# Optimization experiments

Hardware: AMD Instinct MI355X
Metric: run time of the kernel (lower is better)

The kernel has to match this reference:

```python
import jax, jax.numpy as jnp
import numpy as np

D_MODEL = 1024
NUM_TILES = 64
TPC = 8                      # tiles_per_cluster
NUM_CLUSTERS = NUM_TILES // TPC
GRID = 16
COMP_H = 256                 # compress hidden = d_model // 4
NUM_KNOTS = 8
EPS_LN = 1e-5


def setup_inputs() -> dict:
    key = jax.random.key(0)
    ks = jax.random.split(key, 12)
    B, T = 4, 4096
    x = jax.random.normal(ks[0], (B, T, D_MODEL), dtype=jnp.float32)
    signatures_raw = jax.random.normal(ks[1], (NUM_TILES, D_MODEL), dtype=jnp.float32) * 0.5
    knot_values = jax.nn.sigmoid(jnp.linspace(-3.0, 3.0, NUM_KNOTS).astype(jnp.float32))
    temperature = jnp.ones((1,), dtype=jnp.float32)
    # compress: Linear(d,comp_h) -> GELU -> Linear(comp_h,2) -> Tanh
    compress_w1 = jax.random.normal(ks[2], (D_MODEL, COMP_H), dtype=jnp.float32) * (1.0 / np.sqrt(D_MODEL))
    compress_b1 = jnp.zeros((COMP_H,), dtype=jnp.float32)
    compress_w2 = jax.random.normal(ks[3], (COMP_H, 2), dtype=jnp.float32) * (1.0 / np.sqrt(COMP_H))
    compress_b2 = jnp.zeros((2,), dtype=jnp.float32)
    # per-tile magnitude splines: Linear(2,grid) -> ReLU -> Linear(grid,1)
    spline_w1 = jax.random.normal(ks[4], (NUM_TILES, 2, GRID), dtype=jnp.float32) * (1.0 / np.sqrt(2.0))
    spline_b1 = jnp.zeros((NUM_TILES, GRID), dtype=jnp.float32)
    spline_w2 = jax.random.normal(ks[5], (NUM_TILES, GRID, 1), dtype=jnp.float32) * (1.0 / np.sqrt(GRID))
    spline_b2 = jnp.zeros((NUM_TILES, 1), dtype=jnp.float32)
    directions = jax.random.normal(ks[6], (NUM_TILES, D_MODEL), dtype=jnp.float32) * 0.02
    norm_gamma = jnp.ones((D_MODEL,), dtype=jnp.float32)
    norm_beta = jnp.zeros((D_MODEL,), dtype=jnp.float32)
    output_scale = jnp.ones((1,), dtype=jnp.float32) * 0.1
    return dict(x=x, signatures_raw=signatures_raw, knot_values=knot_values,
                temperature=temperature, compress_w1=compress_w1, compress_b1=compress_b1,
                compress_w2=compress_w2, compress_b2=compress_b2, spline_w1=spline_w1,
                spline_b1=spline_b1, spline_w2=spline_w2, spline_b2=spline_b2,
                directions=directions, norm_gamma=norm_gamma, norm_beta=norm_beta,
                output_scale=output_scale)


def _calibrate(scores, knots, temperature):
    # ScoreCalibrationSpline: sigmoid -> linear interpolation over knots
    K = knots.shape[0]
    normalized = jax.nn.sigmoid(scores / (temperature[0] + 1e-6))
    idx_float = normalized * (K - 1)
    idx_low = jnp.clip(idx_float.astype(jnp.int32), 0, K - 2)
    idx_high = idx_low + 1
    t = idx_float - idx_low.astype(scores.dtype)
    val_low = knots[idx_low]
    val_high = knots[idx_high]
    return val_low + t * (val_high - val_low)


def _forward(x, signatures_raw, knot_values, temperature, compress_w1, compress_b1,
             compress_w2, compress_b2, spline_w1, spline_b1, spline_w2, spline_b2,
             directions, norm_gamma, norm_beta, output_scale):
    B, T, D = x.shape
    xf = x.reshape(-1, D)  # [N, D]

    # ternary quantized signatures with straight-through estimator
    q = jnp.where(signatures_raw > 0.3, 1.0,
                  jnp.where(signatures_raw < -0.3, -1.0, 0.0)).astype(signatures_raw.dtype)
    sigs = signatures_raw + jax.lax.stop_gradient(q - signatures_raw)  # [NT, D]

    # hierarchical routing: cluster signatures = sign(mean of member sigs)
    cluster_sigs = jnp.sign(sigs.reshape(NUM_CLUSTERS, TPC, D).mean(axis=1))  # [NC, D]
    cluster_scores = xf @ cluster_sigs.T                                       # [N, NC]
    cluster_gates = _calibrate(cluster_scores, knot_values, temperature)
    cluster_idx = jnp.argmax(cluster_gates, axis=-1)                           # [N]

    # within-cluster tile selection (clusters are contiguous blocks of tiles)
    tile_scores = xf @ sigs.T                                                  # [N, NT]
    tile_gates = _calibrate(tile_scores, knot_values, temperature)
    gates_by_cluster = tile_gates.reshape(-1, NUM_CLUSTERS, TPC)
    sel_gates = jnp.take_along_axis(gates_by_cluster, cluster_idx[:, None, None],
                                    axis=1)[:, 0, :]                            # [N, TPC]
    local_idx = jnp.argmax(sel_gates, axis=-1)
    tile_idx = cluster_idx * TPC + local_idx                                    # [N]

    # compress to 2D spline coordinates
    h = jax.nn.gelu(xf @ compress_w1 + compress_b1, approximate=False)
    comp = jnp.tanh(h @ compress_w2 + compress_b2)                              # [N, 2]

    # batched per-token tiny spline MLP (gather selected tile's weights)
    w1 = spline_w1[tile_idx]                                                    # [N, 2, G]
    b1 = spline_b1[tile_idx]                                                    # [N, G]
    hh = jax.nn.relu(jnp.einsum('ni,nig->ng', comp, w1) + b1)                   # [N, G]
    w2 = spline_w2[tile_idx]                                                    # [N, G, 1]
    b2 = spline_b2[tile_idx]                                                    # [N, 1]
    mag = jnp.einsum('ng,ngo->no', hh, w2) + b2                                 # [N, 1]

    ffn_out = mag * directions[tile_idx] * output_scale[0]                      # [N, D]

    # residual + LayerNorm (dropout in eval mode = identity)
    y = xf + ffn_out
    mu = y.mean(axis=-1, keepdims=True)
    var = ((y - mu) ** 2).mean(axis=-1, keepdims=True)
    y = (y - mu) / jnp.sqrt(var + EPS_LN) * norm_gamma + norm_beta
    return y.reshape(B, T, D)


def reference(x, signatures_raw, knot_values, temperature, compress_w1, compress_b1,
              compress_w2, compress_b2, spline_w1, spline_b1, spline_w2, spline_b2,
              directions, norm_gamma, norm_beta, output_scale):
    return _forward(x, signatures_raw, knot_values, temperature, compress_w1, compress_b1,
                    compress_w2, compress_b2, spline_w1, spline_b1, spline_w2, spline_b2,
                    directions, norm_gamma, norm_beta, output_scale)
```

## Files before the change

### kernel.cpp

```cpp
#include <hip/hip_runtime.h>
#include <hip/hip_bf16.h>
#include <cmath>

#define N_TOK 16384
#define DM    1024
#define CH    256
#define SGRID 16
#define NTP   24

typedef __attribute__((ext_vector_type(8))) short short8;
typedef __attribute__((ext_vector_type(4))) float floatx4;

__device__ __forceinline__ unsigned short f2bf(float f) {
  union { float f; unsigned int u; } v; v.f = f;
  unsigned int r = v.u + 0x7FFFu + ((v.u >> 16) & 1u);
  return (unsigned short)(r >> 16);
}

__device__ __forceinline__ short8 cvt8(float4 u, float4 v) {
  union { short8 s; __hip_bfloat162 h[4]; } r;
  r.h[0] = __float22bfloat162_rn(make_float2(u.x, u.y));
  r.h[1] = __float22bfloat162_rn(make_float2(u.z, u.w));
  r.h[2] = __float22bfloat162_rn(make_float2(v.x, v.y));
  r.h[3] = __float22bfloat162_rn(make_float2(v.z, v.w));
  return r.s;
}

__device__ __forceinline__ float bf2f(unsigned short b) {
  union { unsigned int u; float f; } v; v.u = ((unsigned int)b) << 16; return v.f;
}

__device__ __forceinline__ float calibrate(float s, const float* __restrict__ kn, float temp_eff) {
  float nrm = 1.0f / (1.0f + expf(-s / temp_eff));
  float idxf = nrm * 7.0f;
  int il = (int)idxf; if (il > 6) il = 6;
  float tt = idxf - (float)il;
  float lo = kn[il], hi = kn[il + 1];
  return lo + tt * (hi - lo);
}

__global__ __launch_bounds__(256) void prep_kernel(
    const float* __restrict__ sig_raw, const float* __restrict__ w1,
    unsigned short* __restrict__ wsB) {
  __shared__ float Wt[32][260];
  __shared__ float St[64][33];
  int kk = blockIdx.x, tid = threadIdx.x;
  {
    int r = tid >> 3, c0 = (tid & 7) * 32;
    const float* src = w1 + (size_t)(kk * 32 + r) * CH + c0;
#pragma unroll
    for (int i = 0; i < 8; ++i)
      *(float4*)(&Wt[r][c0 + 4 * i]) = *(const float4*)(src + 4 * i);
  }
  {
    int t = tid >> 2, c0 = (tid & 3) * 8;
    const float* src = sig_raw + (size_t)t * DM + kk * 32 + c0;
#pragma unroll
    for (int i = 0; i < 8; ++i) {
      float rr = src[i];
      St[t][c0 + i] = (rr > 0.3f) ? 1.f : ((rr < -0.3f) ? -1.f : 0.f);
    }
  }
  __syncthreads();
#pragma unroll
  for (int i = 0; i < 4; ++i) {
    int idx = i * 256 + tid;
    int nt = idx >> 6, lane = idx & 63;
    int q = lane >> 4, l = lane & 15;
    short8 v;
#pragma unroll
    for (int j = 0; j < 8; ++j) v[j] = (short)f2bf(Wt[q * 8 + j][nt * 16 + l]);
    *(short8*)(wsB + ((size_t)(kk * NTP + nt) * 64 + lane) * 8) = v;
  }
#pragma unroll
  for (int i = 0; i < 2; ++i) {
    int idx = i * 256 + tid;
    if (idx < 320) {
      int nt = 16 + (idx >> 6), lane = idx & 63;
      int q = lane >> 4, l = lane & 15;
      int n = nt * 16 + l;
      short8 v;
#pragma unroll
      for (int j = 0; j < 8; ++j) {
        int kl = q * 8 + j;
        float val = 0.f;
        if (n < 264) {
          float s = 0.f;
#pragma unroll
          for (int m = 0; m < 8; ++m) s += St[(n - 256) * 8 + m][kl];
          val = (s > 0.f) ? 1.f : ((s < 0.f) ? -1.f : 0.f);
        } else if (n < 328) {
          val = St[n - 264][kl];
        }
        v[j] = (short)f2bf(val);
      }
      *(short8*)(wsB + ((size_t)(kk * NTP + nt) * 64 + lane) * 8) = v;
    }
  }
}


#define LOADK(XBASE, kk, b0, b2r, av)                                       \
  {                                                                         \
    const char* bp = bBase + (size_t)(kk) * (NTP * 1024);                   \
    b0 = *(const short8*)(bp);                                              \
    if (wave < 5) b2r = *(const short8*)(bp + 16384);                       \
    unsigned cpos = ((unsigned)((kk) * 4 + quad) ^ sw) << 3;                \
    _Pragma("unroll") for (int mt = 0; mt < 2; ++mt)                        \
        av[mt] = *(const short8*)((XBASE) + mt * 16384 + arow + cpos);      \
  }

#define COMPUTE(b0, b2r, av)                                                \
  {                                                                         \
    _Pragma("unroll") for (int mt = 0; mt < 2; ++mt)                        \
      acc0[mt] = __builtin_amdgcn_mfma_f32_16x16x32_bf16(av[mt], b0, acc0[mt], 0, 0, 0); \
    if (wave < 5) {                                                         \
      _Pragma("unroll") for (int mt = 0; mt < 2; ++mt)                      \
        acc2[mt] = __builtin_amdgcn_mfma_f32_16x16x32_bf16(av[mt], b2r, acc2[mt], 0, 0, 0); \
    }                                                                       \
  }

#define KLOOP(XBASE)                                                        \
  {                                                                         \
    _Pragma("unroll") for (int mt = 0; mt < 2; ++mt) {                      \
      acc0[mt] = (floatx4){0.f, 0.f, 0.f, 0.f};                             \
      acc2[mt] = (floatx4){0.f, 0.f, 0.f, 0.f};                             \
    }                                                                       \
    LOADK(XBASE, 0, bA0, bA2, aA);                                          \
    _Pragma("unroll 1") for (int kk = 0; kk < 30; kk += 2) {                \
      LOADK(XBASE, kk + 1, bB0, bB2, aB_);                                  \
      COMPUTE(bA0, bA2, aA);                                                \
      LOADK(XBASE, kk + 2, bA0, bA2, aA);                                   \
      COMPUTE(bB0, bB2, aB_);                                               \
    }                                                                       \
    LOADK(XBASE, 31, bB0, bB2, aB_);                                        \
    COMPUTE(bA0, bA2, aA);                                                  \
    COMPUTE(bB0, bB2, aB_);                                                 \
    if (wave < 5) {                                                         \
      int sc = wave * 16 + l15;                                             \
      if (sc < 72) {                                                        \
        _Pragma("unroll") for (int mt = 0; mt < 2; ++mt)                    \
          _Pragma("unroll") for (int r = 0; r < 4; ++r)                     \
            Ssc[mt * 16 + quad * 4 + r][sc] = acc2[mt][r];                  \
      }                                                                     \
    }                                                                       \
    {                                                                       \
      float q0[2][4], q1[2][4];                                             \
      _Pragma("unroll") for (int mt = 0; mt < 2; ++mt)                      \
        _Pragma("unroll") for (int r = 0; r < 4; ++r) {                     \
          float hh = acc0[mt][r] + b1c;                                     \
          hh = 0.5f * hh * (1.0f + erff(hh * 0.7071067811865475f));         \
          q0[mt][r] = hh * w20;                                             \
          q1[mt][r] = hh * w21;                                             \
        }                                                                   \
      _Pragma("unroll") for (int m = 1; m < 16; m <<= 1)                    \
        _Pragma("unroll") for (int mt = 0; mt < 2; ++mt)                    \
          _Pragma("unroll") for (int r = 0; r < 4; ++r) {                   \
            q0[mt][r] += __shfl_xor(q0[mt][r], m);                          \
            q1[mt][r] += __shfl_xor(q1[mt][r], m);                          \
          }                                                                 \
      if (l15 == 0) {                                                       \
        _Pragma("unroll") for (int mt = 0; mt < 2; ++mt)                    \
          _Pragma("unroll") for (int r = 0; r < 4; ++r) {                   \
            Psh[wave][mt * 16 + quad * 4 + r][0] = q0[mt][r];               \
            Psh[wave][mt * 16 + quad * 4 + r][1] = q1[mt][r];               \
          }                                                                 \
      }                                                                     \
    }                                                                       \
  }

#define STWRITE(XBASE, RV)                                                  \
  _Pragma("unroll") for (int i = 0; i < 4; ++i) {                           \
    int cg = tid + 1024 * i;                                                \
    int row = cg >> 7, cir = cg & 127;                                      \
    int pos = cir ^ (row & 7);                                              \
    *(short8*)((XBASE) + row * 1024 + pos * 8) = cvt8(RV[2 * i], RV[2 * i + 1]); \
  }

#define ROUTE()                                                             \
  if (tid < 32) {                                                           \
    int row = tid;                                                          \
    float s0 = b2[0], s1 = b2[1];                                           \
    _Pragma("unroll") for (int j = 0; j < 16; ++j) {                        \
      s0 += Psh[j][row][0];                                                 \
      s1 += Psh[j][row][1];                                                 \
    }                                                                       \
    float c0 = tanhf(s0), c1 = tanhf(s1);                                   \
    float temp_eff = temperature[0] + 1e-6f;                                \
    int cid = 0; float best = -1e30f;                                       \
    _Pragma("unroll") for (int c = 0; c < 8; ++c) {                         \
      float g = calibrate(Ssc[row][c], knots, temp_eff);                    \
      if (g > best) { best = g; cid = c; }                                  \
    }                                                                       \
    int lidx = 0; best = -1e30f;                                            \
    _Pragma("unroll") for (int j = 0; j < 8; ++j) {                         \
      float g = calibrate(Ssc[row][8 + cid * 8 + j], knots, temp_eff);      \
      if (g > best) { best = g; lidx = j; }                                 \
    }                                                                       \
    int t = cid * 8 + lidx;                                                 \
    float mag = sb2[t];                                                     \
    _Pragma("unroll") for (int g2 = 0; g2 < SGRID; ++g2) {                  \
      float hv = c0 * sw1[t * 32 + g2] + c1 * sw1[t * 32 + 16 + g2] + sb1[t * 16 + g2]; \
      hv = fmaxf(hv, 0.f);                                                  \
      mag += hv * sw2[t * 16 + g2];                                         \
    }                                                                       \
    ScaleS[row] = mag * oscale[0];                                          \
    TidxS[row] = t;                                                         \
  }

#define LNOUT(XBASE, TOKBASE)                                               \
  _Pragma("unroll 1") for (int rr = 0; rr < 2; ++rr) {                      \
    int row = wave * 2 + rr;                                                \
    int r7 = row & 7;                                                       \
    float scale = ScaleS[row];                                              \
    const float* dr = dirs + (size_t)TidxS[row] * DM + lane * 16;           \
    const unsigned short* xrow = (XBASE) + row * 1024;                      \
    short8 h0 = *(const short8*)(xrow + (unsigned)((2 * lane) ^ r7) * 8);   \
    short8 h1 = *(const short8*)(xrow + (unsigned)((2 * lane + 1) ^ r7) * 8); \
    float fv[16];                                                           \
    float ssum = 0.f, ssq = 0.f;                                            \
    _Pragma("unroll") for (int i = 0; i < 4; ++i) {                         \
      float4 d4 = *(const float4*)(dr + 4 * i);                             \
      float xa = bf2f((unsigned short)((i < 2 ? h0[i * 4 + 0] : h1[(i - 2) * 4 + 0]))); \
      float xb = bf2f((unsigned short)((i < 2 ? h0[i * 4 + 1] : h1[(i - 2) * 4 + 1]))); \
      float xc = bf2f((unsigned short)((i < 2 ? h0[i * 4 + 2] : h1[(i - 2) * 4 + 2]))); \
      float xd = bf2f((unsigned short)((i < 2 ? h0[i * 4 + 3] : h1[(i - 2) * 4 + 3]))); \
      fv[4 * i + 0] = xa + scale * d4.x;                                    \
      fv[4 * i + 1] = xb + scale * d4.y;                                    \
      fv[4 * i + 2] = xc + scale * d4.z;                                    \
      fv[4 * i + 3] = xd + scale * d4.w;                                    \
      ssum += fv[4 * i + 0] + fv[4 * i + 1] + fv[4 * i + 2] + fv[4 * i + 3]; \
      ssq += fv[4 * i + 0] * fv[4 * i + 0] + fv[4 * i + 1] * fv[4 * i + 1]  \
           + fv[4 * i + 2] * fv[4 * i + 2] + fv[4 * i + 3] * fv[4 * i + 3]; \
    }                                                                       \
    _Pragma("unroll") for (int m = 1; m < 64; m <<= 1) {                    \
      ssum += __shfl_xor(ssum, m);                                          \
      ssq += __shfl_xor(ssq, m);                                            \
    }                                                                       \
    float mu = ssum * (1.0f / 1024.0f);                                     \
    float var = ssq * (1.0f / 1024.0f) - mu * mu;                           \
    float inv = rsqrtf(var + 1e-5f);                                        \
    float* orow = out + (size_t)((TOKBASE) + row) * DM + lane * 16;         \
    const float* gp = gma + lane * 16;                                      \
    const float* bp2 = bta + lane * 16;                                     \
    _Pragma("unroll") for (int i = 0; i < 4; ++i) {                         \
      float4 g4 = *(const float4*)(gp + 4 * i);                             \
      float4 b4 = *(const float4*)(bp2 + 4 * i);                            \
      float4 o;                                                             \
      o.x = (fv[4 * i + 0] - mu) * inv * g4.x + b4.x;                       \
      o.y = (fv[4 * i + 1] - mu) * inv * g4.y + b4.y;                       \
      o.z = (fv[4 * i + 2] - mu) * inv * g4.z + b4.z;                       \
      o.w = (fv[4 * i + 3] - mu) * inv * g4.w + b4.w;                       \
      *(float4*)(orow + 4 * i) = o;                                         \
    }                                                                       \
  }

__global__ __launch_bounds__(1024, 4) void fused_kernel(
    const float* __restrict__ x, const unsigned short* __restrict__ wsB,
    const float* __restrict__ b1v, const float* __restrict__ w2,
    const float* __restrict__ b2, const float* __restrict__ knots,
    const float* __restrict__ temperature, const float* __restrict__ sw1,
    const float* __restrict__ sb1, const float* __restrict__ sw2,
    const float* __restrict__ sb2, const float* __restrict__ dirs,
    const float* __restrict__ gma, const float* __restrict__ bta,
    const float* __restrict__ oscale, float* __restrict__ out) {
  __shared__ unsigned short Xsh[2][32 * 1024];
  __shared__ float Ssc[32][73];
  __shared__ float Psh[16][32][2];
  __shared__ float ScaleS[32];
  __shared__ int   TidxS[32];

  int tid = threadIdx.x;
  int wave = tid >> 6, lane = tid & 63, quad = lane >> 4, l15 = lane & 15;
  int m0 = blockIdx.x * 64;

  const float* base = x + (size_t)m0 * DM;
  float4 ra[8], rb[8];
#pragma unroll
  for (int i = 0; i < 4; ++i) {
    int cg = tid + 1024 * i;
    ra[2 * i]     = *(const float4*)(base + cg * 8);
    ra[2 * i + 1] = *(const float4*)(base + cg * 8 + 4);
  }
#pragma unroll
  for (int i = 0; i < 4; ++i) {
    int cg = tid + 1024 * i;
    rb[2 * i]     = *(const float4*)(base + 32768 + cg * 8);
    rb[2 * i + 1] = *(const float4*)(base + 32768 + cg * 8 + 4);
  }
  __builtin_amdgcn_sched_barrier(0);

  STWRITE(&Xsh[0][0], ra);
  __syncthreads();

  int colC = wave * 16 + l15;
  float b1c = b1v[colC], w20 = w2[2 * colC], w21 = w2[2 * colC + 1];

  floatx4 acc0[2], acc2[2];
  const char* bBase = (const char*)wsB + wave * 1024 + lane * 16;
  int arow = l15 * 1024;
  unsigned sw = (unsigned)(l15 & 7);
  short8 bA0, bA2, bB0, bB2, aA[2], aB_[2];

  KLOOP(&Xsh[0][0]);
  __syncthreads();

  STWRITE(&Xsh[1][0], rb);
  ROUTE();
  __syncthreads();

  LNOUT(&Xsh[0][0], m0);

  KLOOP(&Xsh[1][0]);
  __syncthreads();

  ROUTE();
  __syncthreads();

  LNOUT(&Xsh[1][0], m0 + 32);
}

extern "C" void kernel_launch(void* const* d_in, const int* in_sizes, int n_in,
                              void* d_out, int out_size, void* d_ws, size_t ws_size,
                              hipStream_t stream) {
  const float* x      = (const float*)d_in[0];
  const float* sigraw = (const float*)d_in[1];
  const float* knots  = (const float*)d_in[2];
  const float* temp   = (const float*)d_in[3];
  const float* cw1    = (const float*)d_in[4];
  const float* cb1    = (const float*)d_in[5];
  const float* cw2    = (const float*)d_in[6];
  const float* cb2    = (const float*)d_in[7];
  const float* sw1    = (const float*)d_in[8];
  const float* sb1    = (const float*)d_in[9];
  const float* sw2    = (const float*)d_in[10];
  const float* sb2    = (const float*)d_in[11];
  const float* dirs   = (const float*)d_in[12];
  const float* gma    = (const float*)d_in[13];
  const float* bta    = (const float*)d_in[14];
  const float* oscale = (const float*)d_in[15];
  float* out = (float*)d_out;

  unsigned short* wsB = (unsigned short*)d_ws;

  hipLaunchKernelGGL(prep_kernel, dim3(32), dim3(256), 0, stream,
                     sigraw, cw1, wsB);
  hipLaunchKernelGGL(fused_kernel, dim3(N_TOK / 64), dim3(1024), 0, stream,
                     x, wsB, cb1, cw2, cb2, knots, temp,
                     sw1, sb1, sw2, sb2, dirs, gma, bta, oscale, out);
}
```

Baseline: 182.9 us.

## Split block into two wave groups pipelining stage, GEMM, route and LayerNorm

Splits the 16 waves into two groups of 8 that each own one 32-token half. While one group runs the compress/score MFMA loop, the other stages its half of x into LDS, and later the route and LayerNorm phases of one half overlap the other half's work. Each wave now covers two hidden-column tiles, so only 8 waves share the B operand. This is meant to hide global-load latency behind MFMA work and shorten the serial phase chain. In exchange, only half the waves do MFMA at any moment, register use per wave goes up, and the score and partial-sum buffers in shared memory are doubled.

```diff
diff --git a/kernel.cpp b/kernel.cpp
--- a/kernel.cpp
+++ b/kernel.cpp
@@ -100,58 +100,84 @@
 }
 
 
-#define LOADK(XBASE, kk, b0, b2r, av)                                       \
+#define LOADK(XB, kk, b0, b1, b2r, av)                                      \
   {                                                                         \
     const char* bp = bBase + (size_t)(kk) * (NTP * 1024);                   \
     b0 = *(const short8*)(bp);                                              \
-    if (wave < 5) b2r = *(const short8*)(bp + 16384);                       \
+    b1 = *(const short8*)(bp + 8192);                                       \
+    if (wg < 5) b2r = *(const short8*)(bp + 16384);                         \
     unsigned cpos = ((unsigned)((kk) * 4 + quad) ^ sw) << 3;                \
     _Pragma("unroll") for (int mt = 0; mt < 2; ++mt)                        \
-        av[mt] = *(const short8*)((XBASE) + mt * 16384 + arow + cpos);      \
-  }
-
-#define COMPUTE(b0, b2r, av)                                                \
+        av[mt] = *(const short8*)((XB) + mt * 16384 + arow + cpos);         \
+  }
+
+#define COMPUTE(b0, b1, b2r, av)                                            \
   {                                                                         \
-    _Pragma("unroll") for (int mt = 0; mt < 2; ++mt)                        \
+    _Pragma("unroll") for (int mt = 0; mt < 2; ++mt) {                      \
       acc0[mt] = __builtin_amdgcn_mfma_f32_16x16x32_bf16(av[mt], b0, acc0[mt], 0, 0, 0); \
-    if (wave < 5) {                                                         \
+      acc1[mt] = __builtin_amdgcn_mfma_f32_16x16x32_bf16(av[mt], b1, acc1[mt], 0, 0, 0); \
+    }                                                                       \
+    if (wg < 5) {                                                           \
       _Pragma("unroll") for (int mt = 0; mt < 2; ++mt)                      \
         acc2[mt] = __builtin_amdgcn_mfma_f32_16x16x32_bf16(av[mt], b2r, acc2[mt], 0, 0, 0); \
     }                                                                       \
   }
 
-#define KLOOP(XBASE)                                                        \
+#define STAGE(G)                                                            \
   {                                                                         \
+    const float* baseg = x + (size_t)(m0 + (G) * 32) * DM;                  \
+    _Pragma("unroll") for (int i2 = 0; i2 < 8; ++i2) {                      \
+      int cg = gt + 512 * i2;                                               \
+      float4 p = *(const float4*)(baseg + cg * 8);                          \
+      float4 q = *(const float4*)(baseg + cg * 8 + 4);                      \
+      int row = cg >> 7, cir = cg & 127;                                    \
+      int pos = cir ^ (row & 7);                                            \
+      *(short8*)(&Xsh[G][row * 1024 + pos * 8]) = cvt8(p, q);               \
+    }                                                                       \
+  }
+
+#define KLOOP(G)                                                            \
+  {                                                                         \
+    floatx4 acc0[2], acc1[2], acc2[2];                                      \
     _Pragma("unroll") for (int mt = 0; mt < 2; ++mt) {                      \
       acc0[mt] = (floatx4){0.f, 0.f, 0.f, 0.f};                             \
+      acc1[mt] = (floatx4){0.f, 0.f, 0.f, 0.f};                             \
       acc2[mt] = (floatx4){0.f, 0.f, 0.f, 0.f};                             \
     }                                                                       \
-    LOADK(XBASE, 0, bA0, bA2, aA);                                          \
+    const unsigned short* XB = &Xsh[G][0];                                  \
+    short8 bA0, bA1, bA2, bB0, bB1, bB2, aA[2], aB_[2];                     \
+    LOADK(XB, 0, bA0, bA1, bA2, aA);                                        \
     _Pragma("unroll 1") for (int kk = 0; kk < 30; kk += 2) {                \
-      LOADK(XBASE, kk + 1, bB0, bB2, aB_);                                  \
-      COMPUTE(bA0, bA2, aA);                                                \
-      LOADK(XBASE, kk + 2, bA0, bA2, aA);                                   \
-      COMPUTE(bB0, bB2, aB_);                                               \
-    }                                                                       \
-    LOADK(XBASE, 31, bB0, bB2, aB_);                                        \
-    COMPUTE(bA0, bA2, aA);                                                  \
-    COMPUTE(bB0, bB2, aB_);                                                 \
-    if (wave < 5) {                                                         \
-      int sc = wave * 16 + l15;                                             \
+      LOADK(XB, kk + 1, bB0, bB1, bB2, aB_);                                \
+      COMPUTE(bA0, bA1, bA2, aA);                                           \
+      LOADK(XB, kk + 2, bA0, bA1, bA2, aA);                                 \
+      COMPUTE(bB0, bB1, bB2, aB_);                                          \
+    }                                                                       \
+    LOADK(XB, 31, bB0, bB1, bB2, aB_);                                      \
+    COMPUTE(bA0, bA1, bA2, aA);                                             \
+    COMPUTE(bB0, bB1, bB2, aB_);                                            \
+    if (wg < 5) {                                                           \
+      int sc = wg * 16 + l15;                                               \
       if (sc < 72) {                                                        \
         _Pragma("unroll") for (int mt = 0; mt < 2; ++mt)                    \
           _Pragma("unroll") for (int r = 0; r < 4; ++r)                     \
-            Ssc[mt * 16 + quad * 4 + r][sc] = acc2[mt][r];                  \
+            Ssc[G][mt * 16 + quad * 4 + r][sc] = acc2[mt][r];               \
       }                                                                     \
     }                                                                       \
     {                                                                       \
+      int colA = wg * 16 + l15;                                             \
+      int colB = 128 + wg * 16 + l15;                                       \
+      float b1cA = b1v[colA], w20A = w2[2 * colA], w21A = w2[2 * colA + 1]; \
+      float b1cB = b1v[colB], w20B = w2[2 * colB], w21B = w2[2 * colB + 1]; \
       float q0[2][4], q1[2][4];                                             \
       _Pragma("unroll") for (int mt = 0; mt < 2; ++mt)                      \
         _Pragma("unroll") for (int r = 0; r < 4; ++r) {                     \
-          float hh = acc0[mt][r] + b1c;                                     \
-          hh = 0.5f * hh * (1.0f + erff(hh * 0.7071067811865475f));         \
-          q0[mt][r] = hh * w20;                                             \
-          q1[mt][r] = hh * w21;                                             \
+          float hA = acc0[mt][r] + b1cA;                                    \
+          hA = 0.5f * hA * (1.0f + erff(hA * 0.7071067811865475f));         \
+          float hB = acc1[mt][r] + b1cB;                                    \
+          hB = 0.5f * hB * (1.0f + erff(hB * 0.7071067811865475f));         \
+          q0[mt][r] = hA * w20A + hB * w20B;                                \
+          q1[mt][r] = hA * w21A + hB * w21B;                                \
         }                                                                   \
       _Pragma("unroll") for (int m = 1; m < 16; m <<= 1)                    \
         _Pragma("unroll") for (int mt = 0; mt < 2; ++mt)                    \
@@ -162,40 +188,32 @@
       if (l15 == 0) {                                                       \
         _Pragma("unroll") for (int mt = 0; mt < 2; ++mt)                    \
           _Pragma("unroll") for (int r = 0; r < 4; ++r) {                   \
-            Psh[wave][mt * 16 + quad * 4 + r][0] = q0[mt][r];               \
-            Psh[wave][mt * 16 + quad * 4 + r][1] = q1[mt][r];               \
+            Psh[G][wg][mt * 16 + quad * 4 + r][0] = q0[mt][r];              \
+            Psh[G][wg][mt * 16 + quad * 4 + r][1] = q1[mt][r];              \
           }                                                                 \
       }                                                                     \
     }                                                                       \
   }
 
-#define STWRITE(XBASE, RV)                                                  \
-  _Pragma("unroll") for (int i = 0; i < 4; ++i) {                           \
-    int cg = tid + 1024 * i;                                                \
-    int row = cg >> 7, cir = cg & 127;                                      \
-    int pos = cir ^ (row & 7);                                              \
-    *(short8*)((XBASE) + row * 1024 + pos * 8) = cvt8(RV[2 * i], RV[2 * i + 1]); \
-  }
-
-#define ROUTE()                                                             \
-  if (tid < 32) {                                                           \
-    int row = tid;                                                          \
+#define ROUTE(G)                                                            \
+  if (wg == 0 && lane < 32) {                                               \
+    int row = lane;                                                         \
     float s0 = b2[0], s1 = b2[1];                                           \
-    _Pragma("unroll") for (int j = 0; j < 16; ++j) {                        \
-      s0 += Psh[j][row][0];                                                 \
-      s1 += Psh[j][row][1];                                                 \
+    _Pragma("unroll") for (int j = 0; j < 8; ++j) {                         \
+      s0 += Psh[G][j][row][0];                                              \
+      s1 += Psh[G][j][row][1];                                              \
     }                                                                       \
     float c0 = tanhf(s0), c1 = tanhf(s1);                                   \
     float temp_eff = temperature[0] + 1e-6f;                                \
     int cid = 0; float best = -1e30f;                                       \
     _Pragma("unroll") for (int c = 0; c < 8; ++c) {                         \
-      float g = calibrate(Ssc[row][c], knots, temp_eff);                    \
-      if (g > best) { best = g; cid = c; }                                  \
+      float g2v = calibrate(Ssc[G][row][c], knots, temp_eff);               \
+      if (g2v > best) { best = g2v; cid = c; }                              \
     }                                                                       \
     int lidx = 0; best = -1e30f;                                            \
     _Pragma("unroll") for (int j = 0; j < 8; ++j) {                         \
-      float g = calibrate(Ssc[row][8 + cid * 8 + j], knots, temp_eff);      \
-      if (g > best) { best = g; lidx = j; }                                 \
+      float g2v = calibrate(Ssc[G][row][8 + cid * 8 + j], knots, temp_eff); \
+      if (g2v > best) { best = g2v; lidx = j; }                             \
     }                                                                       \
     int t = cid * 8 + lidx;                                                 \
     float mag = sb2[t];                                                     \
@@ -204,17 +222,17 @@
       hv = fmaxf(hv, 0.f);                                                  \
       mag += hv * sw2[t * 16 + g2];                                         \
     }                                                                       \
-    ScaleS[row] = mag * oscale[0];                                          \
-    TidxS[row] = t;                                                         \
-  }
-
-#define LNOUT(XBASE, TOKBASE)                                               \
-  _Pragma("unroll 1") for (int rr = 0; rr < 2; ++rr) {                      \
-    int row = wave * 2 + rr;                                                \
+    ScaleS[G][row] = mag * oscale[0];                                       \
+    TidxS[G][row] = t;                                                      \
+  }
+
+#define LNOUT(G)                                                            \
+  _Pragma("unroll 1") for (int rr = 0; rr < 4; ++rr) {                      \
+    int row = wg * 4 + rr;                                                  \
     int r7 = row & 7;                                                       \
-    float scale = ScaleS[row];                                              \
-    const float* dr = dirs + (size_t)TidxS[row] * DM + lane * 16;           \
-    const unsigned short* xrow = (XBASE) + row * 1024;                      \
+    float scale = ScaleS[G][row];                                           \
+    const float* dr = dirs + (size_t)TidxS[G][row] * DM + lane * 16;        \
+    const unsigned short* xrow = &Xsh[G][row * 1024];                       \
     short8 h0 = *(const short8*)(xrow + (unsigned)((2 * lane) ^ r7) * 8);   \
     short8 h1 = *(const short8*)(xrow + (unsigned)((2 * lane + 1) ^ r7) * 8); \
     float fv[16];                                                           \
@@ -240,7 +258,7 @@
     float mu = ssum * (1.0f / 1024.0f);                                     \
     float var = ssq * (1.0f / 1024.0f) - mu * mu;                           \
     float inv = rsqrtf(var + 1e-5f);                                        \
-    float* orow = out + (size_t)((TOKBASE) + row) * DM + lane * 16;         \
+    float* orow = out + (size_t)(m0 + (G) * 32 + row) * DM + lane * 16;     \
     const float* gp = gma + lane * 16;                                      \
     const float* bp2 = bta + lane * 16;                                     \
     _Pragma("unroll") for (int i = 0; i < 4; ++i) {                         \
@@ -265,59 +283,34 @@
     const float* __restrict__ gma, const float* __restrict__ bta,
     const float* __restrict__ oscale, float* __restrict__ out) {
   __shared__ unsigned short Xsh[2][32 * 1024];
-  __shared__ float Ssc[32][73];
-  __shared__ float Psh[16][32][2];
-  __shared__ float ScaleS[32];
-  __shared__ int   TidxS[32];
+  __shared__ float Ssc[2][32][73];
+  __shared__ float Psh[2][8][32][2];
+  __shared__ float ScaleS[2][32];
+  __shared__ int   TidxS[2][32];
 
   int tid = threadIdx.x;
   int wave = tid >> 6, lane = tid & 63, quad = lane >> 4, l15 = lane & 15;
+  int g = wave >> 3, wg = wave & 7;
+  int gt = tid & 511;
   int m0 = blockIdx.x * 64;
 
-  const float* base = x + (size_t)m0 * DM;
-  float4 ra[8], rb[8];
-#pragma unroll
-  for (int i = 0; i < 4; ++i) {
-    int cg = tid + 1024 * i;
-    ra[2 * i]     = *(const float4*)(base + cg * 8);
-    ra[2 * i + 1] = *(const float4*)(base + cg * 8 + 4);
-  }
-#pragma unroll
-  for (int i = 0; i < 4; ++i) {
-    int cg = tid + 1024 * i;
-    rb[2 * i]     = *(const float4*)(base + 32768 + cg * 8);
-    rb[2 * i + 1] = *(const float4*)(base + 32768 + cg * 8 + 4);
-  }
-  __builtin_amdgcn_sched_barrier(0);
-
-  STWRITE(&Xsh[0][0], ra);
-  __syncthreads();
-
-  int colC = wave * 16 + l15;
-  float b1c = b1v[colC], w20 = w2[2 * colC], w21 = w2[2 * colC + 1];
-
-  floatx4 acc0[2], acc2[2];
-  const char* bBase = (const char*)wsB + wave * 1024 + lane * 16;
+  const char* bBase = (const char*)wsB + wg * 1024 + lane * 16;
   int arow = l15 * 1024;
   unsigned sw = (unsigned)(l15 & 7);
-  short8 bA0, bA2, bB0, bB2, aA[2], aB_[2];
-
-  KLOOP(&Xsh[0][0]);
-  __syncthreads();
-
-  STWRITE(&Xsh[1][0], rb);
-  ROUTE();
-  __syncthreads();
-
-  LNOUT(&Xsh[0][0], m0);
-
-  KLOOP(&Xsh[1][0]);
-  __syncthreads();
-
-  ROUTE();
-  __syncthreads();
-
-  LNOUT(&Xsh[1][0], m0 + 32);
+
+  if (g == 0) { STAGE(0); }
+  __syncthreads();
+
+  if (g == 0) { KLOOP(0); } else { STAGE(1); }
+  __syncthreads();
+
+  if (g == 0) { ROUTE(0); } else { KLOOP(1); }
+  __syncthreads();
+
+  if (g == 0) { LNOUT(0); } else { ROUTE(1); }
+  __syncthreads();
+
+  if (g == 1) { LNOUT(1); }
 }
 
 extern "C" void kernel_launch(void* const* d_in, const int* in_sizes, int n_in,
```

After: 177.5 us. -2.9%, faster.
